# Performance work log

Measured on AMD Instinct MI355X. Metric: run time of the kernel, lower is better.

Reference implementation:

```python
import jax, jax.numpy as jnp
import numpy as np

B, T, D, H = 2048, 250, 128, 100

def setup_inputs() -> dict:
    key = jax.random.key(0)
    k1, k2, k3, k4 = jax.random.split(key, 4)
    x = jax.random.normal(k1, (B, T, D), dtype=jnp.float32)
    # fused LSTM kernels, gate order (i, f, g, o); scale for stability
    Wi = jax.random.normal(k2, (D, 4 * H), dtype=jnp.float32) * 0.05
    Wh = jax.random.normal(k3, (H, 4 * H), dtype=jnp.float32) * 0.05
    bh = jnp.zeros((4 * H,), dtype=jnp.float32)
    Wd = jax.random.normal(k4, (H, H), dtype=jnp.float32) * 0.05
    bd = jnp.zeros((H,), dtype=jnp.float32)
    return {"x": x, "Wi": Wi, "Wh": Wh, "bh": bh, "Wd": Wd, "bd": bd}

def reference(x, Wi, Wh, bh, Wd, bd):
    b = x.shape[0]
    # precompute input contribution for all timesteps: [B, T, 4H]
    xz = jnp.einsum('btd,dg->btg', x, Wi) + bh

    def step(carry, xz_t):
        c, h = carry
        z = xz_t + h @ Wh                      # [B, 4H]
        i, f, g, o = jnp.split(z, 4, axis=-1)  # flax gate order i,f,g,o
        i = jax.nn.sigmoid(i)
        f = jax.nn.sigmoid(f)
        g = jnp.tanh(g)
        o = jax.nn.sigmoid(o)
        c = f * c + i * g
        h = o * jnp.tanh(c)
        return (c, h), h

    c0 = jnp.zeros((b, H), dtype=x.dtype)
    h0 = jnp.zeros((b, H), dtype=x.dtype)
    _, hs = jax.lax.scan(step, (c0, h0), jnp.swapaxes(xz, 0, 1))
    hs = jnp.swapaxes(hs, 0, 1)                # [B, T, H]
    return jax.nn.relu(hs @ Wd + bd)
```

## Files before the change

### kernel.cpp

```cpp
#include <hip/hip_runtime.h>

#define TPB 512

typedef __attribute__((ext_vector_type(8))) short bf16x8;
typedef __attribute__((ext_vector_type(4))) float f32x4;

__device__ __forceinline__ short f2bf(float f) {
    union { float f; unsigned u; } v; v.f = f;
    unsigned r = (v.u + 0x7FFFu + ((v.u >> 16) & 1u)) >> 16;
    return (short)r;
}

__device__ __forceinline__ float frcp(float x) {
#if __has_builtin(__builtin_amdgcn_rcpf)
    return __builtin_amdgcn_rcpf(x);
#else
    return 1.0f / x;
#endif
}

__device__ __forceinline__ float fast_sig(float x) {
    return frcp(1.0f + __expf(-x));
}
__device__ __forceinline__ float fast_tanh(float x) {
    return 1.0f - 2.0f * frcp(1.0f + __expf(2.0f * x));
}

__device__ __forceinline__ float permlane_pack(float a, float b) {
#if __has_builtin(__builtin_amdgcn_permlane32_swap)
    auto r = __builtin_amdgcn_permlane32_swap(__float_as_int(a), __float_as_int(b),
                                              false, false);
    return __int_as_float(r[0]);
#else
    const int l  = (int)(threadIdx.x & 63);
    const int bs = __shfl(__float_as_int(b), l ^ 32, 64);
    return __int_as_float(l >= 32 ? bs : __float_as_int(a));
#endif
}

__device__ __forceinline__ void block_sync_lds() {
    asm volatile("s_waitcnt lgkmcnt(0)\n\ts_barrier" ::: "memory");
}

__global__ __launch_bounds__(TPB, 2) void lstm_fused_all(
    const float* __restrict__ x,
    const float* __restrict__ Wi,
    const float* __restrict__ Wh,
    const float* __restrict__ bh,
    const float* __restrict__ Wd,
    const float* __restrict__ bd,
    float* __restrict__ out)
{
    const int tid  = threadIdx.x;
    const int lane = tid & 63;
    const int wave = tid >> 6;
    const int m16  = lane & 15;
    const int kg   = lane >> 4;
    const int b0   = blockIdx.x * 8;

    __shared__ short xA[2][16 * 136];
    __shared__ short hA[2][16 * 136];

    for (int i = tid; i < 2 * 16 * 136; i += TPB) ((short*)xA)[i] = 0;
    for (int i = tid; i < 2 * 16 * 136; i += TPB) ((short*)hA)[i] = 0;

    const int  cg    = wave * 16 + m16;
    const bool valid = (cg < 100);

    bf16x8 bWi[4][4], bWh[4][4], bWd[4];
    float  bhv[4];
    #pragma unroll
    for (int G = 0; G < 4; ++G) {
        const int c = G * 100 + cg;
        bhv[G] = valid ? bh[c] : 0.0f;
        #pragma unroll
        for (int s = 0; s < 4; ++s) {
            bf16x8 vi, vh;
            #pragma unroll
            for (int j = 0; j < 8; ++j) {
                const int k = s * 32 + kg * 8 + j;
                vi[j] = f2bf(valid ? Wi[k * 400 + c] : 0.0f);
                vh[j] = f2bf((valid && k < 100) ? Wh[k * 400 + c] : 0.0f);
            }
            bWi[G][s] = vi;
            bWh[G][s] = vh;
        }
    }
    const float bdv = valid ? bd[cg] : 0.0f;
    #pragma unroll
    for (int s = 0; s < 4; ++s) {
        bf16x8 vd;
        #pragma unroll
        for (int j = 0; j < 8; ++j) {
            const int k = s * 32 + kg * 8 + j;
            vd[j] = f2bf((valid && k < 100) ? Wd[k * 100 + cg] : 0.0f);
        }
        bWd[s] = vd;
    }

    const int kgq     = (lane >> 4) & 1;
    const int rowbase = kgq * 4 + ((lane >= 32) ? 2 : 0);
    float myC[2] = {0.f, 0.f};
    long  ob2[2];
    #pragma unroll
    for (int j = 0; j < 2; ++j)
        ob2[j] = (long)(b0 + rowbase + j) * 25000 + cg;

    const long xbase = ((long)(b0 + wave) * 250) * 128 + lane * 2;
    float2 xp = *(const float2*)&x[xbase];

    const int aoff = m16 * 136 + kg * 8;

    __syncthreads();

    #pragma unroll 1
    for (int t = 0; t <= 250; ++t) {
        const int buf = t & 1;
        if (t < 250) {
            short2 s2; s2.x = f2bf(xp.x); s2.y = f2bf(xp.y);
            *(short2*)&xA[buf][wave * 136 + lane * 2] = s2;
        }
        block_sync_lds();

        if (t + 1 < 250)
            xp = *(const float2*)&x[xbase + (long)(t + 1) * 128];

        bf16x8 aH[4];
        #pragma unroll
        for (int s = 0; s < 4; ++s)
            aH[s] = *(const bf16x8*)&hA[buf][aoff + s * 32];

        if (t < 250) {
            bf16x8 aX[4];
            #pragma unroll
            for (int s = 0; s < 4; ++s)
                aX[s] = *(const bf16x8*)&xA[buf][aoff + s * 32];

            f32x4 accH0[4], accH1[4];
            #pragma unroll
            for (int G = 0; G < 4; ++G) {
                const f32x4 zz = {0.f, 0.f, 0.f, 0.f};
                accH0[G] = __builtin_amdgcn_mfma_f32_16x16x32_bf16(aH[0], bWh[G][0], zz, 0, 0, 0);
                accH1[G] = __builtin_amdgcn_mfma_f32_16x16x32_bf16(aH[2], bWh[G][2], zz, 0, 0, 0);
            }
            #pragma unroll
            for (int G = 0; G < 4; ++G) {
                accH0[G] = __builtin_amdgcn_mfma_f32_16x16x32_bf16(aH[1], bWh[G][1], accH0[G], 0, 0, 0);
                accH1[G] = __builtin_amdgcn_mfma_f32_16x16x32_bf16(aH[3], bWh[G][3], accH1[G], 0, 0, 0);
            }

            f32x4 accI[4];
            #pragma unroll
            for (int G = 0; G < 4; ++G) {
                const f32x4 a = {bhv[G], bhv[G], bhv[G], bhv[G]};
                accI[G] = a;
            }
            #pragma unroll
            for (int s = 0; s < 4; ++s) {
                #pragma unroll
                for (int G = 0; G < 4; ++G)
                    accI[G] = __builtin_amdgcn_mfma_f32_16x16x32_bf16(aX[s], bWi[G][s], accI[G], 0, 0, 0);
            }

            float z0[4], z1[4];
            #pragma unroll
            for (int G = 0; G < 4; ++G) {
                const f32x4 zs = accI[G] + (accH0[G] + accH1[G]);
                z0[G] = permlane_pack(zs[0], zs[2]);
                z1[G] = permlane_pack(zs[1], zs[3]);
            }
            if (valid) {
                {
                    const float ig = fast_sig(z0[0]);
                    const float fg = fast_sig(z0[1]);
                    const float gg = fast_tanh(z0[2]);
                    const float og = fast_sig(z0[3]);
                    const float cs = fg * myC[0] + ig * gg;
                    myC[0] = cs;
                    const float h = og * fast_tanh(cs);
                    hA[buf ^ 1][(rowbase + 0) * 136 + cg] = f2bf(h);
                }
                {
                    const float ig = fast_sig(z1[0]);
                    const float fg = fast_sig(z1[1]);
                    const float gg = fast_tanh(z1[2]);
                    const float og = fast_sig(z1[3]);
                    const float cs = fg * myC[1] + ig * gg;
                    myC[1] = cs;
                    const float h = og * fast_tanh(cs);
                    hA[buf ^ 1][(rowbase + 1) * 136 + cg] = f2bf(h);
                }
            }
        }

        if (t > 0) {
            f32x4 oacc = {bdv, bdv, bdv, bdv};
            #pragma unroll
            for (int s = 0; s < 4; ++s)
                oacc = __builtin_amdgcn_mfma_f32_16x16x32_bf16(aH[s], bWd[s], oacc, 0, 0, 0);
            const float o0 = permlane_pack(oacc[0], oacc[2]);
            const float o1 = permlane_pack(oacc[1], oacc[3]);
            if (valid) {
                out[ob2[0] + (long)(t - 1) * 100] = o0 > 0.0f ? o0 : 0.0f;
                out[ob2[1] + (long)(t - 1) * 100] = o1 > 0.0f ? o1 : 0.0f;
            }
        }
    }
}

extern "C" void kernel_launch(void* const* d_in, const int* in_sizes, int n_in,
                              void* d_out, int out_size, void* d_ws, size_t ws_size,
                              hipStream_t stream) {
    (void)in_sizes; (void)n_in; (void)out_size; (void)d_ws; (void)ws_size;
    const float* x  = (const float*)d_in[0];
    const float* Wi = (const float*)d_in[1];
    const float* Wh = (const float*)d_in[2];
    const float* bh = (const float*)d_in[3];
    const float* Wd = (const float*)d_in[4];
    const float* bd = (const float*)d_in[5];
    float* out = (float*)d_out;

    lstm_fused_all<<<256, TPB, 0, stream>>>(x, Wi, Wh, bh, Wd, bd, out);
}
```

Measured before the change: 798.8 us.

## Drop eighth wave, precompute next-step input projection off the recurrent critical path

Block size drops from 8 to 7 waves, since the eighth wave's gate columns (112..127) were all beyond H=100. Wave 0 now also loads the eighth batch row of x. The input-projection MFMAs for step t+1 are issued after the step-t gate update rather than before it, moving them off the h-dependent critical path. A third x LDS buffer and a two-deep register prefetch of x support this. It adds register pressure (accI held across iterations) and extra work on wave 0, and output offsets become running counters.

After: 679.7 us. 1.18x faster.

```diff
diff --git a/kernel.cpp b/kernel.cpp
--- a/kernel.cpp
+++ b/kernel.cpp
@@ -1,6 +1,6 @@
 #include <hip/hip_runtime.h>
 
-#define TPB 512
+#define TPB 448
 
 typedef __attribute__((ext_vector_type(8))) short bf16x8;
 typedef __attribute__((ext_vector_type(4))) float f32x4;
@@ -58,10 +58,10 @@
     const int kg   = lane >> 4;
     const int b0   = blockIdx.x * 8;
 
-    __shared__ short xA[2][16 * 136];
+    __shared__ short xA[3][16 * 136];
     __shared__ short hA[2][16 * 136];
 
-    for (int i = tid; i < 2 * 16 * 136; i += TPB) ((short*)xA)[i] = 0;
+    for (int i = tid; i < 3 * 16 * 136; i += TPB) ((short*)xA)[i] = 0;
     for (int i = tid; i < 2 * 16 * 136; i += TPB) ((short*)hA)[i] = 0;
 
     const int  cg    = wave * 16 + m16;
@@ -106,36 +106,80 @@
     for (int j = 0; j < 2; ++j)
         ob2[j] = (long)(b0 + rowbase + j) * 25000 + cg;
 
-    const long xbase = ((long)(b0 + wave) * 250) * 128 + lane * 2;
-    float2 xp = *(const float2*)&x[xbase];
+    const long xb0 = ((long)(b0 + wave) * 250) * 128 + lane * 2;
+    const long xb1 = ((long)(b0 + 7)    * 250) * 128 + lane * 2;
+    float2 la0, la1 = {0.f, 0.f}, lb0, lb1 = {0.f, 0.f};
+    la0 = *(const float2*)&x[xb0];
+    if (wave == 0) la1 = *(const float2*)&x[xb1];
+    lb0 = *(const float2*)&x[xb0 + 128];
+    if (wave == 0) lb1 = *(const float2*)&x[xb1 + 128];
 
     const int aoff = m16 * 136 + kg * 8;
 
     __syncthreads();
+
+    {
+        short2 s0; s0.x = f2bf(la0.x); s0.y = f2bf(la0.y);
+        *(short2*)&xA[0][wave * 136 + lane * 2] = s0;
+        if (wave == 0) {
+            short2 s1; s1.x = f2bf(la1.x); s1.y = f2bf(la1.y);
+            *(short2*)&xA[0][7 * 136 + lane * 2] = s1;
+        }
+    }
+    __syncthreads();
+    la0 = lb0; if (wave == 0) la1 = lb1;
+    lb0 = *(const float2*)&x[xb0 + 2 * 128];
+    if (wave == 0) lb1 = *(const float2*)&x[xb1 + 2 * 128];
+
+    f32x4 accI[4];
+    {
+        bf16x8 aX[4];
+        #pragma unroll
+        for (int s = 0; s < 4; ++s)
+            aX[s] = *(const bf16x8*)&xA[0][aoff + s * 32];
+        #pragma unroll
+        for (int G = 0; G < 4; ++G) {
+            const f32x4 a = {bhv[G], bhv[G], bhv[G], bhv[G]};
+            accI[G] = a;
+        }
+        #pragma unroll
+        for (int s = 0; s < 4; ++s)
+            #pragma unroll
+            for (int G = 0; G < 4; ++G)
+                accI[G] = __builtin_amdgcn_mfma_f32_16x16x32_bf16(aX[s], bWi[G][s], accI[G], 0, 0, 0);
+    }
+
+    int  bufx = 1;
+    int  ooff = 0;
+    long xoff = 3 * 128;
 
     #pragma unroll 1
     for (int t = 0; t <= 250; ++t) {
-        const int buf = t & 1;
+        const int bufh = t & 1;
+
+        if (t + 1 < 250) {
+            short2 s0; s0.x = f2bf(la0.x); s0.y = f2bf(la0.y);
+            *(short2*)&xA[bufx][wave * 136 + lane * 2] = s0;
+            if (wave == 0) {
+                short2 s1; s1.x = f2bf(la1.x); s1.y = f2bf(la1.y);
+                *(short2*)&xA[bufx][7 * 136 + lane * 2] = s1;
+            }
+        }
+        block_sync_lds();
+
+        if (t + 1 < 250) { la0 = lb0; if (wave == 0) la1 = lb1; }
+        if (t + 3 < 250) {
+            lb0 = *(const float2*)&x[xb0 + xoff];
+            if (wave == 0) lb1 = *(const float2*)&x[xb1 + xoff];
+        }
+        xoff += 128;
+
+        bf16x8 aH[4];
+        #pragma unroll
+        for (int s = 0; s < 4; ++s)
+            aH[s] = *(const bf16x8*)&hA[bufh][aoff + s * 32];
+
         if (t < 250) {
-            short2 s2; s2.x = f2bf(xp.x); s2.y = f2bf(xp.y);
-            *(short2*)&xA[buf][wave * 136 + lane * 2] = s2;
-        }
-        block_sync_lds();
-
-        if (t + 1 < 250)
-            xp = *(const float2*)&x[xbase + (long)(t + 1) * 128];
-
-        bf16x8 aH[4];
-        #pragma unroll
-        for (int s = 0; s < 4; ++s)
-            aH[s] = *(const bf16x8*)&hA[buf][aoff + s * 32];
-
-        if (t < 250) {
-            bf16x8 aX[4];
-            #pragma unroll
-            for (int s = 0; s < 4; ++s)
-                aX[s] = *(const bf16x8*)&xA[buf][aoff + s * 32];
-
             f32x4 accH0[4], accH1[4];
             #pragma unroll
             for (int G = 0; G < 4; ++G) {
@@ -147,19 +191,6 @@
             for (int G = 0; G < 4; ++G) {
                 accH0[G] = __builtin_amdgcn_mfma_f32_16x16x32_bf16(aH[1], bWh[G][1], accH0[G], 0, 0, 0);
                 accH1[G] = __builtin_amdgcn_mfma_f32_16x16x32_bf16(aH[3], bWh[G][3], accH1[G], 0, 0, 0);
-            }
-
-            f32x4 accI[4];
-            #pragma unroll
-            for (int G = 0; G < 4; ++G) {
-                const f32x4 a = {bhv[G], bhv[G], bhv[G], bhv[G]};
-                accI[G] = a;
-            }
-            #pragma unroll
-            for (int s = 0; s < 4; ++s) {
-                #pragma unroll
-                for (int G = 0; G < 4; ++G)
-                    accI[G] = __builtin_amdgcn_mfma_f32_16x16x32_bf16(aX[s], bWi[G][s], accI[G], 0, 0, 0);
             }
 
             float z0[4], z1[4];
@@ -178,7 +209,7 @@
                     const float cs = fg * myC[0] + ig * gg;
                     myC[0] = cs;
                     const float h = og * fast_tanh(cs);
-                    hA[buf ^ 1][(rowbase + 0) * 136 + cg] = f2bf(h);
+                    hA[bufh ^ 1][(rowbase + 0) * 136 + cg] = f2bf(h);
                 }
                 {
                     const float ig = fast_sig(z1[0]);
@@ -188,9 +219,27 @@
                     const float cs = fg * myC[1] + ig * gg;
                     myC[1] = cs;
                     const float h = og * fast_tanh(cs);
-                    hA[buf ^ 1][(rowbase + 1) * 136 + cg] = f2bf(h);
+                    hA[bufh ^ 1][(rowbase + 1) * 136 + cg] = f2bf(h);
                 }
             }
+        }
+
+        if (t + 1 < 250) {
+            bf16x8 aX[4];
+            #pragma unroll
+            for (int s = 0; s < 4; ++s)
+                aX[s] = *(const bf16x8*)&xA[bufx][aoff + s * 32];
+            #pragma unroll
+            for (int G = 0; G < 4; ++G) {
+                const f32x4 a = {bhv[G], bhv[G], bhv[G], bhv[G]};
+                accI[G] = a;
+            }
+            #pragma unroll
+            for (int s = 0; s < 4; ++s)
+                #pragma unroll
+                for (int G = 0; G < 4; ++G)
+                    accI[G] = __builtin_amdgcn_mfma_f32_16x16x32_bf16(aX[s], bWi[G][s], accI[G], 0, 0, 0);
+            bufx = (bufx == 2) ? 0 : bufx + 1;
         }
 
         if (t > 0) {
@@ -201,9 +250,10 @@
             const float o0 = permlane_pack(oacc[0], oacc[2]);
             const float o1 = permlane_pack(oacc[1], oacc[3]);
             if (valid) {
-                out[ob2[0] + (long)(t - 1) * 100] = o0 > 0.0f ? o0 : 0.0f;
-                out[ob2[1] + (long)(t - 1) * 100] = o1 > 0.0f ? o1 : 0.0f;
-            }
+                out[ob2[0] + ooff] = o0 > 0.0f ? o0 : 0.0f;
+                out[ob2[1] + ooff] = o1 > 0.0f ? o1 : 0.0f;
+            }
+            ooff += 100;
         }
     }
 }
```
